# Optimization experiments

Measured on AMD Instinct MI355X. Metric: run time of the kernel, lower is better.

The kernel has to match this reference:

```python
import jax, jax.numpy as jnp
import numpy as np

N = 50000        # num graph nodes
E = 800000       # num edges (before self-loops)
IN_DIM = 128     # input feature dim
HID = 32         # hidden dim per head
HEADS1 = 4       # gat1 heads (concat)
AGENTS = 32      # num_agents
NEG_SLOPE = 0.2  # PyG GATConv default leaky_relu slope


def setup_inputs() -> dict:
    key = jax.random.key(0)
    ks = jax.random.split(key, 16)
    s = 0.1
    x = jax.random.normal(ks[0], (N, IN_DIM), jnp.float32)
    edge_index = jax.random.randint(ks[1], (2, E), 0, N, dtype=jnp.int64)
    # GATConv layer 1: in=128 -> heads=4, out=32 (concat -> 128)
    W1 = jax.random.normal(ks[2], (IN_DIM, HEADS1 * HID), jnp.float32) * s
    a1s = jax.random.normal(ks[3], (HEADS1, HID), jnp.float32) * s
    a1d = jax.random.normal(ks[4], (HEADS1, HID), jnp.float32) * s
    b1 = jnp.zeros((HEADS1 * HID,), jnp.float32)
    # GATConv layer 2: in=128 -> heads=1, out=32
    W2 = jax.random.normal(ks[5], (HEADS1 * HID, 1 * HID), jnp.float32) * s
    a2s = jax.random.normal(ks[6], (1, HID), jnp.float32) * s
    a2d = jax.random.normal(ks[7], (1, HID), jnp.float32) * s
    b2 = jnp.zeros((HID,), jnp.float32)
    # actor / critic heads
    Wa = jax.random.normal(ks[8], (HID, AGENTS), jnp.float32) * s
    ba = jnp.zeros((AGENTS,), jnp.float32)
    Wc = jax.random.normal(ks[9], (HID, 1), jnp.float32) * s
    bc = jnp.zeros((1,), jnp.float32)
    return {"x": x, "edge_index": edge_index,
            "W1": W1, "a1s": a1s, "a1d": a1d, "b1": b1,
            "W2": W2, "a2s": a2s, "a2d": a2d, "b2": b2,
            "Wa": Wa, "ba": ba, "Wc": Wc, "bc": bc}


def gat_layer(x, edge_index, W, a_src, a_dst, b, heads, out_ch):
    """PyG-style GATConv: self-loops, per-edge attention, segment softmax over
    incoming edges of each target node, scatter-add aggregation, concat heads."""
    n = x.shape[0]
    loop = jnp.arange(n, dtype=edge_index.dtype)
    src = jnp.concatenate([edge_index[0], loop])  # message source j
    dst = jnp.concatenate([edge_index[1], loop])  # message target i
    h = (x @ W).reshape(n, heads, out_ch)                     # [N,H,F]
    a_s = jnp.sum(h * a_src, axis=-1)                         # [N,H]
    a_d = jnp.sum(h * a_dst, axis=-1)                         # [N,H]
    e = jax.nn.leaky_relu(a_s[src] + a_d[dst], NEG_SLOPE)     # [E',H]
    m = jax.ops.segment_max(e, dst, num_segments=n)           # per-target max
    ex = jnp.exp(e - m[dst])
    den = jax.ops.segment_sum(ex, dst, num_segments=n)
    alpha = ex / den[dst]                                     # [E',H]
    out = jax.ops.segment_sum(alpha[:, :, None] * h[src], dst, num_segments=n)
    return out.reshape(n, heads * out_ch) + b


def reference(x, edge_index, W1, a1s, a1d, b1, W2, a2s, a2d, b2, Wa, ba, Wc, bc):
    h = jax.nn.elu(gat_layer(x, edge_index, W1, a1s, a1d, b1, HEADS1, HID))
    h = jax.nn.elu(gat_layer(h, edge_index, W2, a2s, a2d, b2, 1, HID))
    logits = (h @ Wa + ba).T            # [AGENTS, N]
    value = (h @ Wc + bc).mean(axis=0)  # [1]
    return logits, value
```

## Files before the change

### kernel.cpp

```cpp
#include <hip/hip_runtime.h>
#include <math.h>


#define TILE 4096

typedef __attribute__((ext_vector_type(8))) short short8;
typedef __attribute__((ext_vector_type(4))) float floatx4;

__device__ __forceinline__ float leaky02(float e){ return e > 0.f ? e : 0.2f*e; }

__device__ __forceinline__ unsigned short f2bf(float f){
    union { float f; unsigned int i; } v; v.f = f;
    unsigned int r = v.i + 0x7fffu + ((v.i >> 16) & 1u);
    return (unsigned short)(r >> 16);
}
__device__ __forceinline__ float bfx(unsigned int g){
    union { unsigned int i; float f; } v; v.i = g << 16; return v.f;
}
__device__ __forceinline__ float bfy(unsigned int g){
    union { unsigned int i; float f; } v; v.i = g & 0xffff0000u; return v.f;
}
__device__ __forceinline__ float bf1(unsigned short u){
    union { unsigned int i; float f; } v; v.i = ((unsigned int)u) << 16; return v.f;
}

__global__ void k_prep(const float* __restrict__ W1, const float* __restrict__ W2,
                       unsigned short* __restrict__ w1t, unsigned short* __restrict__ w2t)
{
    int tid = threadIdx.x;
    for (int i = tid; i < 128*128; i += 256){
        int nn = i >> 7, k = i & 127;
        w1t[i] = f2bf(W1[k*128 + nn]);
    }
    for (int i = tid; i < 32*128; i += 256){
        int nn = i >> 7, k = i & 127;
        w2t[i] = f2bf(W2[k*32 + nn]);
    }
}

__global__ __launch_bounds__(256) void k_cnt(const int* __restrict__ ei, int e, int e2,
                                             int* __restrict__ counts)
{
    __shared__ int h[256];
    int t = threadIdx.x;
    h[t] = 0; __syncthreads();
    int base = blockIdx.x*TILE;
    #pragma unroll
    for (int k = 0; k < TILE/256; k++){
        int i = base + k*256 + t;
        if (i < e2){
            int d = (i < e) ? ei[(size_t)e + i] : (i - e);
            atomicAdd(&h[d >> 8], 1);
        }
    }
    __syncthreads();
    counts[blockIdx.x*256 + t] = h[t];
}

__global__ void k_base(int* __restrict__ counts, int nb, int* __restrict__ base257,
                       float* __restrict__ out_val, const float* __restrict__ bc)
{
    __shared__ int sb[256];
    int t = threadIdx.x;
    if (t == 0) *out_val = bc[0];
    int running = 0;
    for (int b = 0; b < nb; b++){
        int c = counts[b*256 + t];
        counts[b*256 + t] = running;
        running += c;
    }
    sb[t] = running; __syncthreads();
    for (int off = 1; off < 256; off <<= 1){
        int v = (t >= off) ? sb[t-off] : 0;
        __syncthreads();
        if (t >= off) sb[t] += v;
        __syncthreads();
    }
    base257[t] = sb[t] - running;
    if (t == 255) base257[256] = sb[t];
}

__global__ __launch_bounds__(256) void k_bucket(const int* __restrict__ ei, int e, int e2,
        const int* __restrict__ counts, const int* __restrict__ base257,
        unsigned int* __restrict__ buck)
{
    __shared__ int curs[256];
    int t = threadIdx.x;
    curs[t] = counts[blockIdx.x*256 + t] + base257[t];
    __syncthreads();
    int base = blockIdx.x*TILE;
    #pragma unroll
    for (int k = 0; k < TILE/256; k++){
        int i = base + k*256 + t;
        if (i < e2){
            int s, d;
            if (i < e){ s = ei[i]; d = ei[(size_t)e + i]; }
            else      { s = i - e; d = i - e; }
            int p = atomicAdd(&curs[d >> 8], 1);
            buck[p] = ((unsigned int)d << 16) | (unsigned int)s;
        }
    }
}

__global__ __launch_bounds__(256) void k_p2(const unsigned int* __restrict__ buck,
        const int* __restrict__ base257, int n,
        int* __restrict__ csr, int* __restrict__ rs, int* __restrict__ re)
{
    __shared__ int bins[256], sc[256], curs[256];
    const int b = blockIdx.x, t = threadIdx.x;
    const int lo = base257[b], hi = base257[b+1];
    bins[t] = 0; __syncthreads();
    for (int i = lo + t; i < hi; i += 256){
        int dg = (buck[i] >> 16) & 0xFF;
        atomicAdd(&bins[dg], 1);
    }
    __syncthreads();
    sc[t] = bins[t]; __syncthreads();
    for (int off = 1; off < 256; off <<= 1){
        int v = (t >= off) ? sc[t-off] : 0;
        __syncthreads();
        if (t >= off) sc[t] += v;
        __syncthreads();
    }
    int sInc = sc[t];
    int node = b*256 + t;
    if (node < n){
        rs[node] = lo + sInc - bins[t];
        re[node] = lo + sInc;
    }
    curs[t] = lo + sInc - bins[t];
    __syncthreads();
    for (int i = lo + t; i < hi; i += 256){
        unsigned int pk = buck[i];
        int p = atomicAdd(&curs[(pk >> 16) & 0xFF], 1);
        csr[p] = (int)(pk & 0xFFFFu);
    }
}

__global__ __launch_bounds__(256) void k_gemm1(const float* __restrict__ x,
        const unsigned short* __restrict__ w1t,
        const float* __restrict__ aS, const float* __restrict__ aD,
        unsigned short* __restrict__ h1b, float* __restrict__ pAS, float* __restrict__ pAD, int n)
{
    __shared__ unsigned short As[64*136];
    __shared__ unsigned short Bs[128*136];
    const int tid  = threadIdx.x;
    const int brow = blockIdx.x*64;

    {
        int row = tid >> 2, cb = (tid & 3)*32;
        bool ok = brow + row < n;
        #pragma unroll
        for (int i=0;i<8;i++){
            float4 v = ok ? *(const float4*)&x[(size_t)(brow+row)*128 + cb + i*4]
                          : make_float4(0.f,0.f,0.f,0.f);
            ushort4 b = make_ushort4(f2bf(v.x),f2bf(v.y),f2bf(v.z),f2bf(v.w));
            *(ushort4*)&As[row*136 + cb + i*4] = b;
        }
    }
    {
        int nn = tid >> 1, kb = (tid & 1)*64;
        #pragma unroll
        for (int i=0;i<8;i++)
            *(uint4*)&Bs[nn*136 + kb + i*8] = *(const uint4*)&w1t[nn*128 + kb + i*8];
    }
    __syncthreads();

    const int wv = tid >> 6, lane = tid & 63;
    const int m = lane & 15, quad = lane >> 4;
    floatx4 acc[8];
    #pragma unroll
    for (int i=0;i<8;i++) acc[i] = (floatx4){0.f,0.f,0.f,0.f};

    #pragma unroll
    for (int kc=0; kc<4; kc++){
        int k0 = kc*32 + quad*8;
        short8 a = *(const short8*)&As[(wv*16+m)*136 + k0];
        #pragma unroll
        for (int ct=0; ct<8; ct++){
            short8 b = *(const short8*)&Bs[(ct*16+m)*136 + k0];
            acc[ct] = __builtin_amdgcn_mfma_f32_16x16x32_bf16(a, b, acc[ct], 0,0,0);
        }
    }
    __syncthreads();

    #pragma unroll
    for (int ct=0; ct<8; ct++){
        #pragma unroll
        for (int r=0;r<4;r++){
            int row = wv*16 + quad*4 + r;
            As[row*128 + ct*16 + m] = f2bf(acc[ct][r]);
        }
    }
    __syncthreads();

    {
        int row = tid >> 2, hd = tid & 3;
        int grow = brow + row;
        if (grow < n){
            float ps=0.f, pd=0.f;
            #pragma unroll
            for (int i=0;i<4;i++){
                uint4 u = *(const uint4*)&As[row*128 + hd*32 + i*8];
                *(uint4*)&h1b[(size_t)grow*128 + hd*32 + i*8] = u;
                unsigned int uw[4] = {u.x,u.y,u.z,u.w};
                #pragma unroll
                for (int j=0;j<4;j++){
                    float c0 = bfx(uw[j]), c1 = bfy(uw[j]);
                    int cc = hd*32 + i*8 + j*2;
                    ps += c0*aS[cc] + c1*aS[cc+1];
                    pd += c0*aD[cc] + c1*aD[cc+1];
                }
            }
            pAS[grow*4+hd] = ps;
            pAD[grow*4+hd] = pd;
        }
    }
}

__global__ __launch_bounds__(256) void k_agg1(const int* __restrict__ rs, const int* __restrict__ re,
        const int* __restrict__ csr, const float* __restrict__ as1, const float* __restrict__ ad1,
        const unsigned short* __restrict__ h1b, const float* __restrict__ b1,
        unsigned short* __restrict__ h1ob, int n)
{
    const int lane = threadIdx.x & 63;
    const int node = blockIdx.x*4 + (threadIdx.x >> 6);
    if (node >= n) return;
    const int h   = lane >> 4;
    const int f   = lane*2;
    const int j16 = lane & 15;
    const int grp = lane & 48;
    const float adv = ad1[node*4 + h];
    const int start = rs[node], end = re[node];
    const unsigned int* hp = (const unsigned int*)h1b + (f >> 1);

    float den = 0.f, ax = 0.f, ay = 0.f;
    int i0 = start;

    for (; i0 + 16 <= end; i0 += 16){
        int sj = csr[i0 + j16];
        float e = __expf(leaky02(as1[sj*4 + h] + adv));
        den += e;
        #pragma unroll
        for (int j = 0; j < 16; j++){
            float ej = __shfl(e,  grp + j, 64);
            int   s2 = __shfl(sj, grp + j, 64);
            unsigned int g = hp[s2*64];
            ax += ej*bfx(g); ay += ej*bfy(g);
        }
    }
    int c = end - i0;
    if (c > 0){
        int jj = (j16 < c) ? j16 : (c-1);
        int sj = csr[i0 + jj];
        float e = __expf(leaky02(as1[sj*4 + h] + adv));
        if (j16 < c) den += e;
        for (int j = 0; j < c; j += 4){
            #pragma unroll
            for (int u = 0; u < 4; u++){
                int je = j + u;
                int jc = (je < c) ? je : (c-1);
                float ej = __shfl(e,  grp + jc, 64);
                int   s2 = __shfl(sj, grp + jc, 64);
                ej = (je < c) ? ej : 0.f;
                unsigned int g = hp[s2*64];
                ax += ej*bfx(g); ay += ej*bfy(g);
            }
        }
    }
    den += __shfl_xor(den, 1, 64);
    den += __shfl_xor(den, 2, 64);
    den += __shfl_xor(den, 4, 64);
    den += __shfl_xor(den, 8, 64);

    float ox = ax/den + b1[f];
    float oy = ay/den + b1[f+1];
    ox = ox > 0.f ? ox : expm1f(ox);
    oy = oy > 0.f ? oy : expm1f(oy);
    unsigned int pk = (unsigned int)f2bf(ox) | ((unsigned int)f2bf(oy) << 16);
    *(unsigned int*)&h1ob[(size_t)node*128 + f] = pk;
}

__global__ __launch_bounds__(256) void k_gemm2(const unsigned short* __restrict__ h1ob,
        const unsigned short* __restrict__ w2t,
        const float* __restrict__ aS, const float* __restrict__ aD,
        unsigned short* __restrict__ h2pb, float* __restrict__ pAS, float* __restrict__ pAD, int n)
{
    __shared__ unsigned short As[64*136];
    __shared__ unsigned short Bs[32*136];
    const int tid  = threadIdx.x;
    const int brow = blockIdx.x*64;

    {
        int row = tid >> 2, cb = (tid & 3)*32;
        bool ok = brow + row < n;
        #pragma unroll
        for (int i=0;i<4;i++){
            uint4 v = ok ? *(const uint4*)&h1ob[(size_t)(brow+row)*128 + cb + i*8]
                         : make_uint4(0,0,0,0);
            *(uint4*)&As[row*136 + cb + i*8] = v;
        }
    }
    {
        int nn = tid >> 3, kb = (tid & 7)*16;
        *(uint4*)&Bs[nn*136 + kb]     = *(const uint4*)&w2t[nn*128 + kb];
        *(uint4*)&Bs[nn*136 + kb + 8] = *(const uint4*)&w2t[nn*128 + kb + 8];
    }
    __syncthreads();

    const int wv = tid >> 6, lane = tid & 63;
    const int m = lane & 15, quad = lane >> 4;
    floatx4 acc[2];
    acc[0] = (floatx4){0.f,0.f,0.f,0.f};
    acc[1] = (floatx4){0.f,0.f,0.f,0.f};

    #pragma unroll
    for (int kc=0; kc<4; kc++){
        int k0 = kc*32 + quad*8;
        short8 a = *(const short8*)&As[(wv*16+m)*136 + k0];
        #pragma unroll
        for (int ct=0; ct<2; ct++){
            short8 b = *(const short8*)&Bs[(ct*16+m)*136 + k0];
            acc[ct] = __builtin_amdgcn_mfma_f32_16x16x32_bf16(a, b, acc[ct], 0,0,0);
        }
    }
    __syncthreads();

    #pragma unroll
    for (int ct=0; ct<2; ct++){
        #pragma unroll
        for (int r=0;r<4;r++){
            int row = wv*16 + quad*4 + r;
            As[row*32 + ct*16 + m] = f2bf(acc[ct][r]);
        }
    }
    __syncthreads();

    if (tid < 64){
        int grow = brow + tid;
        if (grow < n){
            float ps=0.f, pd=0.f;
            #pragma unroll
            for (int i=0;i<4;i++){
                uint4 u = *(const uint4*)&As[tid*32 + i*8];
                *(uint4*)&h2pb[(size_t)grow*32 + i*8] = u;
                unsigned int uw[4] = {u.x,u.y,u.z,u.w};
                #pragma unroll
                for (int j=0;j<4;j++){
                    float c0 = bfx(uw[j]), c1 = bfy(uw[j]);
                    int cc = i*8 + j*2;
                    ps += c0*aS[cc] + c1*aS[cc+1];
                    pd += c0*aD[cc] + c1*aD[cc+1];
                }
            }
            pAS[grow] = ps;
            pAD[grow] = pd;
        }
    }
}

__global__ __launch_bounds__(256) void k_agg2(const int* __restrict__ rs, const int* __restrict__ re,
        const int* __restrict__ csr, const float* __restrict__ as2, const float* __restrict__ ad2,
        const unsigned short* __restrict__ h2pb, const float* __restrict__ b2,
        float* __restrict__ out, int n)
{
    const int lane = threadIdx.x & 63;
    const int node = blockIdx.x*4 + (threadIdx.x >> 6);
    if (node >= n) return;
    const int f    = lane & 31;
    const int half = lane >> 5;
    const int j16  = lane & 15;
    const int grp  = lane & 48;
    const float adv = ad2[node];
    const int start = rs[node], end = re[node];
    const unsigned short* hp = h2pb + f;

    float den = 0.f, acc = 0.f;
    int i0 = start;

    for (; i0 + 16 <= end; i0 += 16){
        int sj = csr[i0 + j16];
        float e = __expf(leaky02(as2[sj] + adv));
        den += e;
        #pragma unroll
        for (int jj = 0; jj < 8; jj++){
            int j = 2*jj + half;
            float ej = __shfl(e,  grp + j, 64);
            int   s2 = __shfl(sj, grp + j, 64);
            acc += ej * bf1(hp[s2*32]);
        }
    }
    int c = end - i0;
    if (c > 0){
        int jj = (j16 < c) ? j16 : (c-1);
        int sj = csr[i0 + jj];
        float e = __expf(leaky02(as2[sj] + adv));
        if (j16 < c) den += e;
        for (int j = half; j < c; j += 8){
            #pragma unroll
            for (int u = 0; u < 4; u++){
                int je = j + 2*u;
                int jc = (je < c) ? je : (c-1);
                float ej = __shfl(e,  grp + (jc & 15), 64);
                int   s2 = __shfl(sj, grp + (jc & 15), 64);
                ej = (je < c) ? ej : 0.f;
                acc += ej * bf1(hp[s2*32]);
            }
        }
    }
    den += __shfl_xor(den, 1, 64);
    den += __shfl_xor(den, 2, 64);
    den += __shfl_xor(den, 4, 64);
    den += __shfl_xor(den, 8, 64);
    acc += __shfl_xor(acc, 32, 64);

    if (half == 0){
        float o = acc/den + b2[f];
        o = o > 0.f ? o : expm1f(o);
        out[(size_t)node*32 + f] = o;
    }
}

__global__ __launch_bounds__(256) void k_head(const float* __restrict__ h2, const float* __restrict__ Wa,
        const float* __restrict__ ba, const float* __restrict__ Wc, int n, float* __restrict__ out)
{
    __shared__ float WaS[1024];
    __shared__ float baS[32], WcS[32];
    int tid = threadIdx.x;
    *(float4*)&WaS[tid*4] = *(const float4*)&Wa[tid*4];
    if (tid < 32){ baS[tid] = ba[tid]; WcS[tid] = Wc[tid]; }
    __syncthreads();

    int nidx = blockIdx.x*256 + tid;
    bool act = nidx < n;
    float hv[32];
    #pragma unroll
    for (int j=0;j<8;j++){
        float4 v = act ? *(const float4*)&h2[(size_t)nidx*32 + j*4] : make_float4(0.f,0.f,0.f,0.f);
        hv[j*4+0]=v.x; hv[j*4+1]=v.y; hv[j*4+2]=v.z; hv[j*4+3]=v.w;
    }
    #pragma unroll
    for (int a=0;a<32;a++){
        float acc = baS[a];
        #pragma unroll
        for (int c=0;c<32;c++) acc += hv[c]*WaS[c*32+a];
        if (act) out[(size_t)a*n + nidx] = acc;
    }
    float v = 0.f;
    #pragma unroll
    for (int c=0;c<32;c++) v += hv[c]*WcS[c];
    #pragma unroll
    for (int msk=1; msk<64; msk<<=1) v += __shfl_xor(v, msk, 64);
    if ((tid & 63) == 0) atomicAdd(&out[(size_t)32*n], v*(1.0f/n));
}

extern "C" void kernel_launch(void* const* d_in, const int* in_sizes, int n_in,
                              void* d_out, int out_size, void* d_ws, size_t ws_size,
                              hipStream_t stream)
{
    const float* x   = (const float*)d_in[0];
    const int*   ei  = (const int*)d_in[1];
    const float* W1  = (const float*)d_in[2];
    const float* a1s = (const float*)d_in[3];
    const float* a1d = (const float*)d_in[4];
    const float* b1  = (const float*)d_in[5];
    const float* W2  = (const float*)d_in[6];
    const float* a2s = (const float*)d_in[7];
    const float* a2d = (const float*)d_in[8];
    const float* b2  = (const float*)d_in[9];
    const float* Wa  = (const float*)d_in[10];
    const float* ba  = (const float*)d_in[11];
    const float* Wc  = (const float*)d_in[12];
    const float* bc  = (const float*)d_in[13];
    float* out = (float*)d_out;

    const int N  = in_sizes[0] / 128;
    const int E  = in_sizes[1] / 2;
    const int E2 = E + N;
    const int nbT = (E2 + TILE - 1) / TILE;
    const int nbB = (N + 255) / 256;

    char* base = (char*)d_ws;
    auto alloc = [&](size_t bytes) -> char* {
        char* p = base; base += (bytes + 255) & ~(size_t)255; return p;
    };
    float* h2     = (float*)alloc((size_t)N*32*4);
    float* as1    = (float*)alloc((size_t)N*4*4);
    float* ad1    = (float*)alloc((size_t)N*4*4);
    float* as2    = (float*)alloc((size_t)N*4);
    float* ad2    = (float*)alloc((size_t)N*4);
    int* counts   = (int*)alloc((size_t)nbT*256*4);
    int* base257  = (int*)alloc(257*4);
    int* rs       = (int*)alloc((size_t)N*4);
    int* re       = (int*)alloc((size_t)N*4);
    int* csr      = (int*)alloc((size_t)E2*4);
    unsigned int* buck = (unsigned int*)alloc((size_t)E2*4);
    unsigned short* h1b  = (unsigned short*)alloc((size_t)N*128*2);
    unsigned short* h1ob = (unsigned short*)alloc((size_t)N*128*2);
    unsigned short* h2pb = (unsigned short*)alloc((size_t)N*32*2);
    unsigned short* w1t  = (unsigned short*)alloc(128*128*2);
    unsigned short* w2t  = (unsigned short*)alloc(32*128*2);

    const int nbN   = (N + 255) / 256;
    const int nbG   = (N + 63) / 64;
    const int nbAgg = (N + 3) / 4;

    k_prep<<<1, 256, 0, stream>>>(W1, W2, w1t, w2t);
    k_cnt<<<nbT, 256, 0, stream>>>(ei, E, E2, counts);
    k_base<<<1, 256, 0, stream>>>(counts, nbT, base257, out + (size_t)32*N, bc);
    k_bucket<<<nbT, 256, 0, stream>>>(ei, E, E2, counts, base257, buck);
    k_p2<<<nbB, 256, 0, stream>>>(buck, base257, N, csr, rs, re);
    k_gemm1<<<nbG, 256, 0, stream>>>(x, w1t, a1s, a1d, h1b, as1, ad1, N);
    k_agg1<<<nbAgg, 256, 0, stream>>>(rs, re, csr, as1, ad1, h1b, b1, h1ob, N);
    k_gemm2<<<nbG, 256, 0, stream>>>(h1ob, w2t, a2s, a2d, h2pb, as2, ad2, N);
    k_agg2<<<nbAgg, 256, 0, stream>>>(rs, re, csr, as2, ad2, h2pb, b2, h2, N);
    k_head<<<nbN, 256, 0, stream>>>(h2, Wa, ba, Wc, N, out);
}
```

Measured before the change: 293.7 us.

## Parallelize bucket-count prefix scan across digits with transposed count layout

Moves the per-bucket exclusive scan over tile counts out of a single-block serial loop and into a 256-block kernel, one block per destination bucket. The counts array is stored digit-major so each block scans its row in a coalesced, parallel way. A small second kernel then scans the per-digit totals to produce bucket bases. This adds one extra launch and strided writes in the count and bucket kernels in exchange for removing a serial loop of about 208 iterations run by one block.

```diff
diff --git a/kernel.cpp b/kernel.cpp
--- a/kernel.cpp
+++ b/kernel.cpp
@@ -39,7 +39,7 @@
 }
 
 __global__ __launch_bounds__(256) void k_cnt(const int* __restrict__ ei, int e, int e2,
-                                             int* __restrict__ counts)
+                                             int* __restrict__ counts, int nbT)
 {
     __shared__ int h[256];
     int t = threadIdx.x;
@@ -54,39 +54,59 @@
         }
     }
     __syncthreads();
-    counts[blockIdx.x*256 + t] = h[t];
-}
-
-__global__ void k_base(int* __restrict__ counts, int nb, int* __restrict__ base257,
-                       float* __restrict__ out_val, const float* __restrict__ bc)
+    counts[(size_t)t*nbT + blockIdx.x] = h[t];
+}
+
+__global__ __launch_bounds__(256) void k_scan_digit(int* __restrict__ counts, int nb,
+                                                    int* __restrict__ digTot)
+{
+    __shared__ int sb[256];
+    const int t = blockIdx.x;
+    const int i = threadIdx.x;
+    int carry = 0;
+    for (int c0 = 0; c0 < nb; c0 += 256){
+        int idx = c0 + i;
+        int v = (idx < nb) ? counts[(size_t)t*nb + idx] : 0;
+        sb[i] = v; __syncthreads();
+        for (int off = 1; off < 256; off <<= 1){
+            int u = (i >= off) ? sb[i-off] : 0;
+            __syncthreads();
+            if (i >= off) sb[i] += u;
+            __syncthreads();
+        }
+        if (idx < nb) counts[(size_t)t*nb + idx] = carry + sb[i] - v;
+        int tot = sb[255];
+        __syncthreads();
+        carry += tot;
+    }
+    if (i == 0) digTot[t] = carry;
+}
+
+__global__ void k_base2(const int* __restrict__ digTot, int* __restrict__ base257,
+                        float* __restrict__ out_val, const float* __restrict__ bc)
 {
     __shared__ int sb[256];
     int t = threadIdx.x;
     if (t == 0) *out_val = bc[0];
-    int running = 0;
-    for (int b = 0; b < nb; b++){
-        int c = counts[b*256 + t];
-        counts[b*256 + t] = running;
-        running += c;
-    }
-    sb[t] = running; __syncthreads();
+    int v = digTot[t];
+    sb[t] = v; __syncthreads();
     for (int off = 1; off < 256; off <<= 1){
-        int v = (t >= off) ? sb[t-off] : 0;
+        int u = (t >= off) ? sb[t-off] : 0;
         __syncthreads();
-        if (t >= off) sb[t] += v;
+        if (t >= off) sb[t] += u;
         __syncthreads();
     }
-    base257[t] = sb[t] - running;
+    base257[t] = sb[t] - v;
     if (t == 255) base257[256] = sb[t];
 }
 
 __global__ __launch_bounds__(256) void k_bucket(const int* __restrict__ ei, int e, int e2,
-        const int* __restrict__ counts, const int* __restrict__ base257,
+        const int* __restrict__ counts, int nbT, const int* __restrict__ base257,
         unsigned int* __restrict__ buck)
 {
     __shared__ int curs[256];
     int t = threadIdx.x;
-    curs[t] = counts[blockIdx.x*256 + t] + base257[t];
+    curs[t] = counts[(size_t)t*nbT + blockIdx.x] + base257[t];
     __syncthreads();
     int base = blockIdx.x*TILE;
     #pragma unroll
@@ -490,6 +510,7 @@
     float* as2    = (float*)alloc((size_t)N*4);
     float* ad2    = (float*)alloc((size_t)N*4);
     int* counts   = (int*)alloc((size_t)nbT*256*4);
+    int* digTot   = (int*)alloc(256*4);
     int* base257  = (int*)alloc(257*4);
     int* rs       = (int*)alloc((size_t)N*4);
     int* re       = (int*)alloc((size_t)N*4);
@@ -506,9 +527,10 @@
     const int nbAgg = (N + 3) / 4;
 
     k_prep<<<1, 256, 0, stream>>>(W1, W2, w1t, w2t);
-    k_cnt<<<nbT, 256, 0, stream>>>(ei, E, E2, counts);
-    k_base<<<1, 256, 0, stream>>>(counts, nbT, base257, out + (size_t)32*N, bc);
-    k_bucket<<<nbT, 256, 0, stream>>>(ei, E, E2, counts, base257, buck);
+    k_cnt<<<nbT, 256, 0, stream>>>(ei, E, E2, counts, nbT);
+    k_scan_digit<<<256, 256, 0, stream>>>(counts, nbT, digTot);
+    k_base2<<<1, 256, 0, stream>>>(digTot, base257, out + (size_t)32*N, bc);
+    k_bucket<<<nbT, 256, 0, stream>>>(ei, E, E2, counts, nbT, base257, buck);
     k_p2<<<nbB, 256, 0, stream>>>(buck, base257, N, csr, rs, re);
     k_gemm1<<<nbG, 256, 0, stream>>>(x, w1t, a1s, a1d, h1b, as1, ad1, N);
     k_agg1<<<nbAgg, 256, 0, stream>>>(rs, re, csr, as1, ad1, h1b, b1, h1ob, N);
```

New measurement: 250.6 us. -14.7%, faster.
